# Performance work log

Measured on AMD Instinct MI355X. Metric: run time of the kernel, lower is better.

The kernel has to match this reference:

```python
import jax, jax.numpy as jnp
import numpy as np

D_MODEL = 512
D_ATTN = 128


def setup_inputs() -> dict:
    key = jax.random.key(0)
    k1, k2, k3, k4, k5 = jax.random.split(key, 5)
    B, N = 4, 4096
    x = jax.random.normal(k1, (B, N, D_MODEL), dtype=jnp.float32)
    key_mask = jnp.ones((B, N, 1), dtype=jnp.float32)
    # nn.Linear params (stored as [in, out] for x @ W)
    W_qkv = jax.random.normal(k2, (D_MODEL, 3 * D_ATTN), dtype=jnp.float32) / np.sqrt(D_MODEL)
    b_qkv = jax.random.normal(k3, (3 * D_ATTN,), dtype=jnp.float32) * 0.01
    W_out = jax.random.normal(k4, (D_ATTN, D_MODEL), dtype=jnp.float32) / np.sqrt(D_ATTN)
    b_out = jax.random.normal(k5, (D_MODEL,), dtype=jnp.float32) * 0.01
    return {"x": x, "key_mask": key_mask, "W_qkv": W_qkv, "b_qkv": b_qkv,
            "W_out": W_out, "b_out": b_out}


def reference(x, key_mask, W_qkv, b_qkv, W_out, b_out):
    # Fused QKV projection: [B, N, 3*d_attn]
    qkv = jnp.einsum('bnd,de->bne', x, W_qkv) + b_qkv
    q, k, v = jnp.split(qkv, 3, axis=-1)  # each [B, N, d_attn]
    d_attn = q.shape[-1]
    scale = 1.0 / np.sqrt(d_attn)
    # Full [B, N, N] score matrix (faithful to original einsum)
    scores = jnp.einsum('bnd,bmd->bnm', q, k)
    # Causal mask applied BEFORE scaling (as in original: mask, then *scale)
    N = x.shape[1]
    causal = jnp.tril(jnp.ones((N, N), dtype=bool))  # True = keep
    scores = jnp.where(causal[None, :, :], scores, -jnp.inf)
    scores = scores * scale
    attn = jax.nn.softmax(scores, axis=-1)  # dropout is identity in eval
    out = jnp.einsum('bnm,bmd->bnd', attn, v)
    out = out * key_mask  # broadcast [B, N, 1]
    out = jnp.einsum('bnd,de->bne', out, W_out) + b_out
    return out
```

## Files before the change

### kernel.cpp

```cpp
#include <hip/hip_runtime.h>
#include <hip/hip_bf16.h>
#include <math.h>

typedef __attribute__((ext_vector_type(4))) float f32x4;
typedef __attribute__((ext_vector_type(4))) float fvec4;
typedef __attribute__((ext_vector_type(8))) short bf16x8_t;
typedef __attribute__((ext_vector_type(4))) short bf16x4_t;

static constexpr int BATCH = 4;
static constexpr int SEQ = 4096;
static constexpr int DM = 512;
static constexpr int DA = 128;
static constexpr int BN = BATCH * SEQ;
static constexpr int IPB = 442;
static constexpr int N_ITEMS = BATCH * IPB;

static __device__ __forceinline__ unsigned short f2bf(float f) {
  unsigned u = __builtin_bit_cast(unsigned, f);
  u += 0x7fffu + ((u >> 16) & 1u);
  return (unsigned short)(u >> 16);
}
static __device__ __forceinline__ float bf2f(unsigned short u) {
  return __builtin_bit_cast(float, ((unsigned)u) << 16);
}
static __device__ __forceinline__ float fexp2(float x) {
#if __has_builtin(__builtin_amdgcn_exp2f)
  return __builtin_amdgcn_exp2f(x);
#else
  return exp2f(x);
#endif
}
static __device__ __forceinline__ unsigned pkbf(float lo, float hi) {
  unsigned r;
  asm("v_cvt_pk_bf16_f32 %0, %1, %2" : "=v"(r) : "v"(lo), "v"(hi));
  return r;
}

#define GLDS16(gsrc, ldst)                                                        \
  __builtin_amdgcn_global_load_lds(                                               \
      (const __attribute__((address_space(1))) void*)(gsrc),                      \
      (__attribute__((address_space(3))) void*)(ldst), 16, 0, 0)

static constexpr float QSC = 0.08838834764831845f * 1.4426950408889634f;

__global__ __launch_bounds__(256) void prep_kernel(
    const float* __restrict__ x, const float* __restrict__ Wqkv,
    const float* __restrict__ Wout, unsigned short* __restrict__ xbf,
    unsigned short* __restrict__ WqT, unsigned short* __restrict__ WoT) {
  long long i = ((long long)blockIdx.x * 256 + threadIdx.x) * 8;
  if (i < (long long)BN * DM) {
    fvec4 a = *(const fvec4*)&x[i];
    fvec4 b = *(const fvec4*)&x[i + 4];
    union { bf16x8_t v; unsigned short u[8]; } pk;
    pk.u[0] = f2bf(a[0]); pk.u[1] = f2bf(a[1]); pk.u[2] = f2bf(a[2]); pk.u[3] = f2bf(a[3]);
    pk.u[4] = f2bf(b[0]); pk.u[5] = f2bf(b[1]); pk.u[6] = f2bf(b[2]); pk.u[7] = f2bf(b[3]);
    *(bf16x8_t*)&xbf[i] = pk.v;
  }
  int t = blockIdx.x * 256 + threadIdx.x;
  if (t < 512 * 384) {
    int k = t / 384, n = t - k * 384;
    WqT[n * 512 + k] = f2bf(Wqkv[t]);
  }
  if (t < 128 * 512) {
    int k = t >> 9, n = t & 511;
    WoT[n * 128 + k] = f2bf(Wout[t]);
  }
}

__global__ __launch_bounds__(512, 4) void qkv_kernel(
    const unsigned short* __restrict__ xbf, const unsigned short* __restrict__ WqT,
    const float* __restrict__ bias, unsigned short* __restrict__ qbf,
    unsigned short* __restrict__ kpk, unsigned short* __restrict__ vpk) {
  __shared__ unsigned short Alds[128 * 64];
  __shared__ unsigned short Blds[128 * 64];

  const int m0 = blockIdx.x * 128;
  const int n0 = blockIdx.y * 128;
  const int tid = threadIdx.x;
  const int wave = tid >> 6, lane = tid & 63;
  const int g = lane >> 4, lr = lane & 15;
  const int wm = wave >> 2, wn = wave & 3;

  const int srow = lane >> 3;
  const int sslot = lane & 7;
  const int sksw = ((sslot ^ srow) * 8);

  f32x4 acc[4][2] = {};

  for (int kb = 0; kb < DM; kb += 64) {
    __syncthreads();
#pragma unroll
    for (int i = 0; i < 2; ++i) {
      int ch = wave * 2 + i;
      GLDS16(&xbf[(size_t)(m0 + ch * 8 + srow) * DM + kb + sksw],
             (char*)Alds + ch * 1024);
      GLDS16(&WqT[(size_t)(n0 + ch * 8 + srow) * DM + kb + sksw],
             (char*)Blds + ch * 1024);
    }
    asm volatile("s_waitcnt vmcnt(0)" ::: "memory");
    __syncthreads();

#pragma unroll
    for (int c2 = 0; c2 < 2; ++c2) {
      bf16x8_t ar[4], br[2];
#pragma unroll
      for (int mi = 0; mi < 4; ++mi) {
        int row = wm * 64 + mi * 16 + lr;
        ar[mi] = *(const bf16x8_t*)&Alds[row * 64 + (((c2 * 4 + g) ^ (row & 7)) * 8)];
      }
#pragma unroll
      for (int ni = 0; ni < 2; ++ni) {
        int row = wn * 32 + ni * 16 + lr;
        br[ni] = *(const bf16x8_t*)&Blds[row * 64 + (((c2 * 4 + g) ^ (row & 7)) * 8)];
      }
#pragma unroll
      for (int mi = 0; mi < 4; ++mi)
#pragma unroll
        for (int ni = 0; ni < 2; ++ni)
          acc[mi][ni] = __builtin_amdgcn_mfma_f32_16x16x32_bf16(ar[mi], br[ni],
                                                                acc[mi][ni], 0, 0, 0);
    }
  }

  if (n0 == 0) {
#pragma unroll
    for (int ni = 0; ni < 2; ++ni) {
      int col = wn * 32 + ni * 16 + lr;
      float bv = bias[col];
#pragma unroll
      for (int mi = 0; mi < 4; ++mi) {
        int tokb = m0 + wm * 64 + mi * 16 + 4 * g;
#pragma unroll
        for (int r = 0; r < 4; ++r)
          qbf[(size_t)(tokb + r) * DA + col] = f2bf((acc[mi][ni][r] + bv) * QSC);
      }
    }
  } else if (n0 == 128) {
#pragma unroll
    for (int ni = 0; ni < 2; ++ni) {
      int kd = wn * 32 + ni * 16 + lr;
      float bv = bias[128 + kd];
      int unit = (kd >> 5) * 4 + ((kd >> 3) & 3);
      int elem = kd & 7;
#pragma unroll
      for (int mi = 0; mi < 4; ++mi) {
        int tokb = m0 + wm * 64 + mi * 16 + 4 * g;
#pragma unroll
        for (int r = 0; r < 4; ++r) {
          int token = tokb + r;
          int tile32 = token >> 5;
          int u = (((token >> 4) & 1) * 16) + unit;
          kpk[(size_t)tile32 * 4096 + u * 128 + (token & 15) * 8 + elem] =
              f2bf(acc[mi][ni][r] + bv);
        }
      }
    }
  } else {
#pragma unroll
    for (int mi = 0; mi < 4; ++mi) {
      int keyb = m0 + wm * 64 + mi * 16 + 4 * g;
      int tile32 = keyb >> 5;
      int kl0 = keyb & 31;
      int gp = (kl0 >> 2) & 3;
      int jhi = kl0 >> 4;
#pragma unroll
      for (int ni = 0; ni < 2; ++ni) {
        int d = wn * 32 + ni * 16 + lr;
        float bv = bias[256 + d];
        union { bf16x4_t v; unsigned short u[4]; } pk;
#pragma unroll
        for (int r = 0; r < 4; ++r) pk.u[r] = f2bf(acc[mi][ni][r] + bv);
        int unit = (d >> 4) * 4 + gp;
        *(bf16x4_t*)&vpk[(size_t)tile32 * 4096 + unit * 128 + (d & 15) * 8 + jhi * 4] =
            pk.v;
      }
    }
  }
}

__global__ __launch_bounds__(256, 5) void attn_kernel(
    const unsigned short* __restrict__ qbf, const unsigned short* __restrict__ kpk,
    const unsigned short* __restrict__ vpk, const float* __restrict__ key_mask,
    unsigned short* __restrict__ part_o, float* __restrict__ part_ml,
    unsigned short* __restrict__ ctx) {
  __shared__ unsigned short KV[2][8192];

  const int flat = blockIdx.x;
  const int b = flat & 3;
  const int idxr = flat >> 2;
  int rem = idxr;
  int qt = 63;
  for (;;) {
    int nc = (qt + 5) / 5;
    if (rem < nc) break;
    rem -= nc;
    --qt;
  }
  const int ci = rem;
  const bool direct = (qt < 5);
  const int key0 = ci * 320;
  const int nkeys = min(320, (qt + 1) * 64 - key0);
  const int nt = nkeys >> 5;

  const int tid = threadIdx.x;
  const int wave = tid >> 6, lane = tid & 63;
  const int g = lane >> 4, lr = lane & 15;
  const int qloc = wave * 16 + lr;

  bf16x8_t qf[4];
  {
    const unsigned short* qb =
        qbf + ((size_t)(b * SEQ + qt * 64 + qloc)) * DA + g * 8;
#pragma unroll
    for (int c = 0; c < 4; ++c) qf[c] = *(const bf16x8_t*)(qb + c * 32);
  }

  f32x4 oacc[8] = {};
  float m_r = -INFINITY, l_r = 0.f;

  const int t32b = b * 128 + ci * 10;
  const unsigned short* ksrc = kpk + (size_t)t32b * 4096 + wave * 1024 + lane * 8;
  const unsigned short* vsrc = vpk + (size_t)t32b * 4096 + wave * 1024 + lane * 8;

#define STAGE(buf, tt)                                                       \
  do {                                                                       \
    char* kd_ = (char*)&KV[buf][0] + wave * 2048;                            \
    char* vd_ = (char*)&KV[buf][4096] + wave * 2048;                         \
    _Pragma("unroll")                                                        \
    for (int i_ = 0; i_ < 2; ++i_) {                                         \
      GLDS16(ksrc + (size_t)(tt) * 4096 + i_ * 512, kd_ + i_ * 1024);        \
      GLDS16(vsrc + (size_t)(tt) * 4096 + i_ * 512, vd_ + i_ * 1024);        \
    }                                                                        \
  } while (0)

  STAGE(0, 0);

  for (int tt = 0; tt < nt; ++tt) {
    const int cur = tt & 1;
    if (tt + 1 < nt) {
      STAGE(cur ^ 1, tt + 1);
      asm volatile("s_waitcnt vmcnt(4)" ::: "memory");
    } else {
      asm volatile("s_waitcnt vmcnt(0)" ::: "memory");
    }
    __builtin_amdgcn_s_barrier();
    __builtin_amdgcn_sched_barrier(0);

    f32x4 sacc[2] = {};
    __builtin_amdgcn_s_setprio(1);
#pragma unroll
    for (int ct = 0; ct < 2; ++ct)
#pragma unroll
      for (int c = 0; c < 4; ++c) {
        bf16x8_t kf = *(const bf16x8_t*)&KV[cur][((ct * 16 + c * 4 + g) * 16 + lr) * 8];
        sacc[ct] = __builtin_amdgcn_mfma_f32_16x16x32_bf16(kf, qf[c], sacc[ct], 0, 0, 0);
      }
    __builtin_amdgcn_s_setprio(0);

    const int koff = key0 + tt * 32 - qt * 64;
    if (koff + 31 > wave * 16) {
      int thr = qloc - koff;
#pragma unroll
      for (int ct = 0; ct < 2; ++ct)
#pragma unroll
        for (int r = 0; r < 4; ++r)
          if (16 * ct + 4 * g + r > thr) sacc[ct][r] = -INFINITY;
    }

    float tmax = fmaxf(fmaxf(fmaxf(sacc[0][0], sacc[0][1]), fmaxf(sacc[0][2], sacc[0][3])),
                       fmaxf(fmaxf(sacc[1][0], sacc[1][1]), fmaxf(sacc[1][2], sacc[1][3])));
    tmax = fmaxf(tmax, __shfl_xor(tmax, 16, 64));
    tmax = fmaxf(tmax, __shfl_xor(tmax, 32, 64));

    if (!__all(tmax <= m_r + 10.0f)) {
      float mn = fmaxf(m_r, tmax);
      float al = fexp2(m_r - mn);
      m_r = mn;
      l_r *= al;
#pragma unroll
      for (int t = 0; t < 8; ++t)
#pragma unroll
        for (int r = 0; r < 4; ++r) oacc[t][r] *= al;
    }

    float rs = 0.f;
#pragma unroll
    for (int ct = 0; ct < 2; ++ct)
#pragma unroll
      for (int r = 0; r < 4; ++r) {
        float p = fexp2(sacc[ct][r] - m_r);
        sacc[ct][r] = p;
        rs += p;
      }
    rs += __shfl_xor(rs, 16, 64);
    rs += __shfl_xor(rs, 32, 64);
    l_r += rs;

    bf16x8_t pb;
    {
      union { unsigned u[4]; bf16x8_t v; } pk;
      pk.u[0] = pkbf(sacc[0][0], sacc[0][1]);
      pk.u[1] = pkbf(sacc[0][2], sacc[0][3]);
      pk.u[2] = pkbf(sacc[1][0], sacc[1][1]);
      pk.u[3] = pkbf(sacc[1][2], sacc[1][3]);
      pb = pk.v;
    }

    __builtin_amdgcn_s_setprio(1);
#pragma unroll
    for (int t = 0; t < 8; ++t) {
      bf16x8_t vf = *(const bf16x8_t*)&KV[cur][4096 + ((t * 4 + g) * 16 + lr) * 8];
      oacc[t] = __builtin_amdgcn_mfma_f32_16x16x32_bf16(vf, pb, oacc[t], 0, 0, 0);
    }
    __builtin_amdgcn_s_setprio(0);

    __builtin_amdgcn_s_barrier();
  }
#undef STAGE

  const int row = qloc;
  if (direct) {
    float km = key_mask[b * SEQ + qt * 64 + row];
    float inv = km / l_r;
    unsigned short* co = ctx + ((size_t)(b * SEQ + qt * 64 + row)) * DA;
#pragma unroll
    for (int t = 0; t < 8; ++t) {
      union { bf16x4_t v; unsigned short u[4]; } pk;
#pragma unroll
      for (int r = 0; r < 4; ++r) pk.u[r] = f2bf(oacc[t][r] * inv);
      *(bf16x4_t*)&co[t * 16 + 4 * g] = pk.v;
    }
  } else {
    const int slot = b * IPB + idxr;
    unsigned short* po = part_o + (size_t)slot * 8192 + row * 128;
#pragma unroll
    for (int t = 0; t < 8; ++t) {
      union { bf16x4_t v; unsigned short u[4]; } pk;
#pragma unroll
      for (int r = 0; r < 4; ++r) pk.u[r] = f2bf(oacc[t][r]);
      *(bf16x4_t*)&po[t * 16 + 4 * g] = pk.v;
    }
    if (g == 0) {
      float2 ml = make_float2(m_r, l_r);
      *(float2*)&part_ml[((size_t)slot * 64 + row) * 2] = ml;
    }
  }
}

__global__ __launch_bounds__(256) void combine_kernel(
    const unsigned short* __restrict__ part_o, const float* __restrict__ part_ml,
    const float* __restrict__ key_mask, unsigned short* __restrict__ ctx) {
  const int qt = 5 + blockIdx.x;
  const int b = blockIdx.y;
  const int nc = (qt + 5) / 5;
  int idx0 = 0;
  for (int q = 63; q > qt; --q) idx0 += (q + 5) / 5;
  const int row = threadIdx.x >> 2, cg = threadIdx.x & 3;

  float m = -INFINITY;
  for (int ci = 0; ci < nc; ++ci) {
    int slot = b * IPB + idx0 + ci;
    m = fmaxf(m, part_ml[((size_t)slot * 64 + row) * 2 + 0]);
  }
  float l = 0.f;
  float acc[32];
#pragma unroll
  for (int k = 0; k < 32; ++k) acc[k] = 0.f;
  for (int ci = 0; ci < nc; ++ci) {
    int slot = b * IPB + idx0 + ci;
    float mi = part_ml[((size_t)slot * 64 + row) * 2 + 0];
    float li = part_ml[((size_t)slot * 64 + row) * 2 + 1];
    float w = fexp2(mi - m);
    l += w * li;
    const unsigned short* po = part_o + (size_t)slot * 8192 + row * 128 + cg * 32;
#pragma unroll
    for (int k8 = 0; k8 < 4; ++k8) {
      bf16x8_t v = *(const bf16x8_t*)(po + k8 * 8);
#pragma unroll
      for (int jj = 0; jj < 8; ++jj)
        acc[k8 * 8 + jj] += w * bf2f((unsigned short)v[jj]);
    }
  }
  int rowg = (b * 64 + qt) * 64 + row;
  float sc = key_mask[rowg] / l;
  unsigned short* co = ctx + (size_t)rowg * 128 + cg * 32;
#pragma unroll
  for (int k8 = 0; k8 < 4; ++k8) {
    union { bf16x8_t v; unsigned short u[8]; } pk;
#pragma unroll
    for (int jj = 0; jj < 8; ++jj) pk.u[jj] = f2bf(acc[k8 * 8 + jj] * sc);
    *(bf16x8_t*)(co + k8 * 8) = pk.v;
  }
}

__global__ __launch_bounds__(256) void outproj_kernel(
    const unsigned short* __restrict__ ctx, const unsigned short* __restrict__ WoT,
    const float* __restrict__ bias, float* __restrict__ out) {
  __shared__ unsigned short Alds[64 * 32];
  __shared__ unsigned short Blds[64 * 32];

  const int m0 = blockIdx.x * 64;
  const int n0 = blockIdx.y * 64;
  const int tid = threadIdx.x;
  const int wave = tid >> 6, lane = tid & 63;
  const int g = lane >> 4, lr = lane & 15;
  const int sar = tid >> 2, sak = tid & 3;
  const int sbc = tid & 63, sbk = tid >> 6;

  f32x4 acc[4] = {};

  for (int kb = 0; kb < DA; kb += 32) {
    __syncthreads();
    {
      bf16x8_t v = *(const bf16x8_t*)&ctx[(size_t)(m0 + sar) * DA + kb + sak * 8];
      *(bf16x8_t*)&Alds[(((sar >> 4) * 4 + sak) * 16 + (sar & 15)) * 8] = v;
    }
    {
      bf16x8_t v = *(const bf16x8_t*)&WoT[(size_t)(n0 + sbc) * DA + kb + sbk * 8];
      *(bf16x8_t*)&Blds[(((sbc >> 4) * 4 + sbk) * 16 + (sbc & 15)) * 8] = v;
    }
    __syncthreads();
    bf16x8_t af = *(const bf16x8_t*)&Alds[((wave * 4 + g) * 16 + lr) * 8];
#pragma unroll
    for (int c = 0; c < 4; ++c) {
      bf16x8_t bfr = *(const bf16x8_t*)&Blds[((c * 4 + g) * 16 + lr) * 8];
      acc[c] = __builtin_amdgcn_mfma_f32_16x16x32_bf16(af, bfr, acc[c], 0, 0, 0);
    }
  }

  const int rowb = m0 + wave * 16 + g * 4;
#pragma unroll
  for (int c = 0; c < 4; ++c) {
    int col = n0 + c * 16 + lr;
    float bv = bias[col];
#pragma unroll
    for (int r = 0; r < 4; ++r)
      out[(size_t)(rowb + r) * DM + col] = acc[c][r] + bv;
  }
}

extern "C" void kernel_launch(void* const* d_in, const int* in_sizes, int n_in,
                              void* d_out, int out_size, void* d_ws, size_t ws_size,
                              hipStream_t stream) {
  const float* x = (const float*)d_in[0];
  const float* key_mask = (const float*)d_in[1];
  const float* W_qkv = (const float*)d_in[2];
  const float* b_qkv = (const float*)d_in[3];
  const float* W_out = (const float*)d_in[4];
  const float* b_out = (const float*)d_in[5];
  float* out = (float*)d_out;

  unsigned short* ws = (unsigned short*)d_ws;
  unsigned short* qbf = ws;
  unsigned short* kpk = qbf + (size_t)BN * DA;
  unsigned short* vpk = kpk + (size_t)BN * DA;
  unsigned short* ctx = vpk + (size_t)BN * DA;
  unsigned short* xbf = ctx + (size_t)BN * DA;
  unsigned short* WqT = xbf + (size_t)BN * DM;
  unsigned short* WoT = WqT + (size_t)384 * 512;
  unsigned short* part_o = WoT + (size_t)512 * 128;
  float* part_ml = (float*)(part_o + (size_t)N_ITEMS * 8192);

  prep_kernel<<<dim3((BN * DM / 8 + 255) / 256), 256, 0, stream>>>(
      x, W_qkv, W_out, xbf, WqT, WoT);
  qkv_kernel<<<dim3(BN / 128, 3), 512, 0, stream>>>(xbf, WqT, b_qkv, qbf, kpk, vpk);
  attn_kernel<<<dim3(N_ITEMS), 256, 0, stream>>>(qbf, kpk, vpk, key_mask,
                                                 part_o, part_ml, ctx);
  combine_kernel<<<dim3(59, 4), 256, 0, stream>>>(part_o, part_ml, key_mask, ctx);
  outproj_kernel<<<dim3(BN / 64, 8), 256, 0, stream>>>(ctx, WoT, b_out, out);
}
```

Before: 89.79 us.

## Process 128 queries per attention block to reuse each staged K/V tile

Each attention workgroup now handles two 64-row query groups (128 queries), so every K/V tile staged into LDS feeds twice as many MFMAs. The split-K work items, partial buffers and combine kernel are resized to match. Mask values switch from -inf to large finite constants so fully masked rows stay finite. The aim is to halve K/V global and LDS traffic per unit of work. In exchange, register pressure doubles, occupancy drops (launch bounds 5 to 2), and there are fewer, larger work items, which may balance poorly across CUs.

```diff
diff --git a/kernel.cpp b/kernel.cpp
--- a/kernel.cpp
+++ b/kernel.cpp
@@ -12,8 +12,11 @@
 static constexpr int DM = 512;
 static constexpr int DA = 128;
 static constexpr int BN = BATCH * SEQ;
-static constexpr int IPB = 442;
+static constexpr int IPB = 224;
 static constexpr int N_ITEMS = BATCH * IPB;
+
+static constexpr float MASKV = -3.0e38f;
+static constexpr float MINIT = -1.0e30f;
 
 static __device__ __forceinline__ unsigned short f2bf(float f) {
   unsigned u = __builtin_bit_cast(unsigned, f);
@@ -178,7 +181,43 @@
   }
 }
 
-__global__ __launch_bounds__(256, 5) void attn_kernel(
+static __device__ __forceinline__ bf16x8_t softmax_grp(
+    f32x4 s[2], float& m_r, float& l_r, f32x4* oacc) {
+  float tmax = fmaxf(fmaxf(fmaxf(s[0][0], s[0][1]), fmaxf(s[0][2], s[0][3])),
+                     fmaxf(fmaxf(s[1][0], s[1][1]), fmaxf(s[1][2], s[1][3])));
+  tmax = fmaxf(tmax, __shfl_xor(tmax, 16, 64));
+  tmax = fmaxf(tmax, __shfl_xor(tmax, 32, 64));
+  if (!__all(tmax <= m_r + 10.0f)) {
+    float mn = fmaxf(m_r, tmax);
+    float al = fexp2(m_r - mn);
+    m_r = mn;
+    l_r *= al;
+#pragma unroll
+    for (int t = 0; t < 8; ++t)
+#pragma unroll
+      for (int r = 0; r < 4; ++r) oacc[t][r] *= al;
+  }
+  float rs = 0.f;
+#pragma unroll
+  for (int ct = 0; ct < 2; ++ct)
+#pragma unroll
+    for (int r = 0; r < 4; ++r) {
+      float p = fexp2(s[ct][r] - m_r);
+      s[ct][r] = p;
+      rs += p;
+    }
+  rs += __shfl_xor(rs, 16, 64);
+  rs += __shfl_xor(rs, 32, 64);
+  l_r += rs;
+  union { unsigned u[4]; bf16x8_t v; } pk;
+  pk.u[0] = pkbf(s[0][0], s[0][1]);
+  pk.u[1] = pkbf(s[0][2], s[0][3]);
+  pk.u[2] = pkbf(s[1][0], s[1][1]);
+  pk.u[3] = pkbf(s[1][2], s[1][3]);
+  return pk.v;
+}
+
+__global__ __launch_bounds__(256, 2) void attn_kernel(
     const unsigned short* __restrict__ qbf, const unsigned short* __restrict__ kpk,
     const unsigned short* __restrict__ vpk, const float* __restrict__ key_mask,
     unsigned short* __restrict__ part_o, float* __restrict__ part_ml,
@@ -189,34 +228,37 @@
   const int b = flat & 3;
   const int idxr = flat >> 2;
   int rem = idxr;
-  int qt = 63;
+  int qb = 31;
   for (;;) {
-    int nc = (qt + 5) / 5;
+    int nc = (2 * (qb + 1) + 4) / 5;
     if (rem < nc) break;
     rem -= nc;
-    --qt;
+    --qb;
   }
   const int ci = rem;
-  const bool direct = (qt < 5);
+  const bool direct = (qb < 2);
   const int key0 = ci * 320;
-  const int nkeys = min(320, (qt + 1) * 64 - key0);
+  const int nkeys = min(320, (qb + 1) * 128 - key0);
   const int nt = nkeys >> 5;
 
   const int tid = threadIdx.x;
   const int wave = tid >> 6, lane = tid & 63;
   const int g = lane >> 4, lr = lane & 15;
-  const int qloc = wave * 16 + lr;
-
-  bf16x8_t qf[4];
+  const int q0 = wave * 16 + lr;
+  const int q1 = q0 + 64;
+
+  bf16x8_t qf0[4], qf1[4];
   {
-    const unsigned short* qb =
-        qbf + ((size_t)(b * SEQ + qt * 64 + qloc)) * DA + g * 8;
-#pragma unroll
-    for (int c = 0; c < 4; ++c) qf[c] = *(const bf16x8_t*)(qb + c * 32);
-  }
-
-  f32x4 oacc[8] = {};
-  float m_r = -INFINITY, l_r = 0.f;
+    const unsigned short* qbase = qbf + ((size_t)(b * SEQ + qb * 128)) * DA + g * 8;
+#pragma unroll
+    for (int c = 0; c < 4; ++c) {
+      qf0[c] = *(const bf16x8_t*)(qbase + (size_t)q0 * DA + c * 32);
+      qf1[c] = *(const bf16x8_t*)(qbase + (size_t)q1 * DA + c * 32);
+    }
+  }
+
+  f32x4 oacc0[8] = {}, oacc1[8] = {};
+  float m0r = MINIT, l0 = 0.f, m1r = MINIT, l1 = 0.f;
 
   const int t32b = b * 128 + ci * 10;
   const unsigned short* ksrc = kpk + (size_t)t32b * 4096 + wave * 1024 + lane * 8;
@@ -246,71 +288,45 @@
     __builtin_amdgcn_s_barrier();
     __builtin_amdgcn_sched_barrier(0);
 
-    f32x4 sacc[2] = {};
+    f32x4 s0[2] = {}, s1[2] = {};
     __builtin_amdgcn_s_setprio(1);
 #pragma unroll
     for (int ct = 0; ct < 2; ++ct)
 #pragma unroll
       for (int c = 0; c < 4; ++c) {
         bf16x8_t kf = *(const bf16x8_t*)&KV[cur][((ct * 16 + c * 4 + g) * 16 + lr) * 8];
-        sacc[ct] = __builtin_amdgcn_mfma_f32_16x16x32_bf16(kf, qf[c], sacc[ct], 0, 0, 0);
+        s0[ct] = __builtin_amdgcn_mfma_f32_16x16x32_bf16(kf, qf0[c], s0[ct], 0, 0, 0);
+        s1[ct] = __builtin_amdgcn_mfma_f32_16x16x32_bf16(kf, qf1[c], s1[ct], 0, 0, 0);
       }
     __builtin_amdgcn_s_setprio(0);
 
-    const int koff = key0 + tt * 32 - qt * 64;
+    const int koff = key0 + tt * 32 - qb * 128;
     if (koff + 31 > wave * 16) {
-      int thr = qloc - koff;
+      int thr = q0 - koff;
 #pragma unroll
       for (int ct = 0; ct < 2; ++ct)
 #pragma unroll
         for (int r = 0; r < 4; ++r)
-          if (16 * ct + 4 * g + r > thr) sacc[ct][r] = -INFINITY;
-    }
-
-    float tmax = fmaxf(fmaxf(fmaxf(sacc[0][0], sacc[0][1]), fmaxf(sacc[0][2], sacc[0][3])),
-                       fmaxf(fmaxf(sacc[1][0], sacc[1][1]), fmaxf(sacc[1][2], sacc[1][3])));
-    tmax = fmaxf(tmax, __shfl_xor(tmax, 16, 64));
-    tmax = fmaxf(tmax, __shfl_xor(tmax, 32, 64));
-
-    if (!__all(tmax <= m_r + 10.0f)) {
-      float mn = fmaxf(m_r, tmax);
-      float al = fexp2(m_r - mn);
-      m_r = mn;
-      l_r *= al;
-#pragma unroll
-      for (int t = 0; t < 8; ++t)
-#pragma unroll
-        for (int r = 0; r < 4; ++r) oacc[t][r] *= al;
-    }
-
-    float rs = 0.f;
-#pragma unroll
-    for (int ct = 0; ct < 2; ++ct)
-#pragma unroll
-      for (int r = 0; r < 4; ++r) {
-        float p = fexp2(sacc[ct][r] - m_r);
-        sacc[ct][r] = p;
-        rs += p;
-      }
-    rs += __shfl_xor(rs, 16, 64);
-    rs += __shfl_xor(rs, 32, 64);
-    l_r += rs;
-
-    bf16x8_t pb;
-    {
-      union { unsigned u[4]; bf16x8_t v; } pk;
-      pk.u[0] = pkbf(sacc[0][0], sacc[0][1]);
-      pk.u[1] = pkbf(sacc[0][2], sacc[0][3]);
-      pk.u[2] = pkbf(sacc[1][0], sacc[1][1]);
-      pk.u[3] = pkbf(sacc[1][2], sacc[1][3]);
-      pb = pk.v;
-    }
+          if (16 * ct + 4 * g + r > thr) s0[ct][r] = MASKV;
+    }
+    if (koff + 31 > 64 + wave * 16) {
+      int thr = q1 - koff;
+#pragma unroll
+      for (int ct = 0; ct < 2; ++ct)
+#pragma unroll
+        for (int r = 0; r < 4; ++r)
+          if (16 * ct + 4 * g + r > thr) s1[ct][r] = MASKV;
+    }
+
+    bf16x8_t pb0 = softmax_grp(s0, m0r, l0, oacc0);
+    bf16x8_t pb1 = softmax_grp(s1, m1r, l1, oacc1);
 
     __builtin_amdgcn_s_setprio(1);
 #pragma unroll
     for (int t = 0; t < 8; ++t) {
       bf16x8_t vf = *(const bf16x8_t*)&KV[cur][4096 + ((t * 4 + g) * 16 + lr) * 8];
-      oacc[t] = __builtin_amdgcn_mfma_f32_16x16x32_bf16(vf, pb, oacc[t], 0, 0, 0);
+      oacc0[t] = __builtin_amdgcn_mfma_f32_16x16x32_bf16(vf, pb0, oacc0[t], 0, 0, 0);
+      oacc1[t] = __builtin_amdgcn_mfma_f32_16x16x32_bf16(vf, pb1, oacc1[t], 0, 0, 0);
     }
     __builtin_amdgcn_s_setprio(0);
 
@@ -318,49 +334,55 @@
   }
 #undef STAGE
 
-  const int row = qloc;
-  if (direct) {
-    float km = key_mask[b * SEQ + qt * 64 + row];
-    float inv = km / l_r;
-    unsigned short* co = ctx + ((size_t)(b * SEQ + qt * 64 + row)) * DA;
-#pragma unroll
-    for (int t = 0; t < 8; ++t) {
-      union { bf16x4_t v; unsigned short u[4]; } pk;
-#pragma unroll
-      for (int r = 0; r < 4; ++r) pk.u[r] = f2bf(oacc[t][r] * inv);
-      *(bf16x4_t*)&co[t * 16 + 4 * g] = pk.v;
-    }
-  } else {
-    const int slot = b * IPB + idxr;
-    unsigned short* po = part_o + (size_t)slot * 8192 + row * 128;
-#pragma unroll
-    for (int t = 0; t < 8; ++t) {
-      union { bf16x4_t v; unsigned short u[4]; } pk;
-#pragma unroll
-      for (int r = 0; r < 4; ++r) pk.u[r] = f2bf(oacc[t][r]);
-      *(bf16x4_t*)&po[t * 16 + 4 * g] = pk.v;
-    }
-    if (g == 0) {
-      float2 ml = make_float2(m_r, l_r);
-      *(float2*)&part_ml[((size_t)slot * 64 + row) * 2] = ml;
-    }
-  }
-}
-
-__global__ __launch_bounds__(256) void combine_kernel(
+  const int slot = b * IPB + idxr;
+#pragma unroll
+  for (int grp = 0; grp < 2; ++grp) {
+    const int row = grp ? q1 : q0;
+    const f32x4* oa = grp ? oacc1 : oacc0;
+    const float mr = grp ? m1r : m0r;
+    const float lr_ = grp ? l1 : l0;
+    if (direct) {
+      float km = key_mask[b * SEQ + qb * 128 + row];
+      float inv = km / lr_;
+      unsigned short* co = ctx + ((size_t)(b * SEQ + qb * 128 + row)) * DA;
+#pragma unroll
+      for (int t = 0; t < 8; ++t) {
+        union { bf16x4_t v; unsigned short u[4]; } pk;
+#pragma unroll
+        for (int r = 0; r < 4; ++r) pk.u[r] = f2bf(oa[t][r] * inv);
+        *(bf16x4_t*)&co[t * 16 + 4 * g] = pk.v;
+      }
+    } else {
+      unsigned short* po = part_o + (size_t)slot * 16384 + (size_t)row * 128;
+#pragma unroll
+      for (int t = 0; t < 8; ++t) {
+        union { bf16x4_t v; unsigned short u[4]; } pk;
+#pragma unroll
+        for (int r = 0; r < 4; ++r) pk.u[r] = f2bf(oa[t][r]);
+        *(bf16x4_t*)&po[t * 16 + 4 * g] = pk.v;
+      }
+      if (g == 0) {
+        float2 ml = make_float2(mr, lr_);
+        *(float2*)&part_ml[((size_t)slot * 128 + row) * 2] = ml;
+      }
+    }
+  }
+}
+
+__global__ __launch_bounds__(512) void combine_kernel(
     const unsigned short* __restrict__ part_o, const float* __restrict__ part_ml,
     const float* __restrict__ key_mask, unsigned short* __restrict__ ctx) {
-  const int qt = 5 + blockIdx.x;
+  const int qb = 2 + blockIdx.x;
   const int b = blockIdx.y;
-  const int nc = (qt + 5) / 5;
+  const int nc = (2 * (qb + 1) + 4) / 5;
   int idx0 = 0;
-  for (int q = 63; q > qt; --q) idx0 += (q + 5) / 5;
+  for (int q = 31; q > qb; --q) idx0 += (2 * (q + 1) + 4) / 5;
   const int row = threadIdx.x >> 2, cg = threadIdx.x & 3;
 
-  float m = -INFINITY;
+  float m = MINIT;
   for (int ci = 0; ci < nc; ++ci) {
     int slot = b * IPB + idx0 + ci;
-    m = fmaxf(m, part_ml[((size_t)slot * 64 + row) * 2 + 0]);
+    m = fmaxf(m, part_ml[((size_t)slot * 128 + row) * 2 + 0]);
   }
   float l = 0.f;
   float acc[32];
@@ -368,11 +390,11 @@
   for (int k = 0; k < 32; ++k) acc[k] = 0.f;
   for (int ci = 0; ci < nc; ++ci) {
     int slot = b * IPB + idx0 + ci;
-    float mi = part_ml[((size_t)slot * 64 + row) * 2 + 0];
-    float li = part_ml[((size_t)slot * 64 + row) * 2 + 1];
+    float mi = part_ml[((size_t)slot * 128 + row) * 2 + 0];
+    float li = part_ml[((size_t)slot * 128 + row) * 2 + 1];
     float w = fexp2(mi - m);
     l += w * li;
-    const unsigned short* po = part_o + (size_t)slot * 8192 + row * 128 + cg * 32;
+    const unsigned short* po = part_o + (size_t)slot * 16384 + (size_t)row * 128 + cg * 32;
 #pragma unroll
     for (int k8 = 0; k8 < 4; ++k8) {
       bf16x8_t v = *(const bf16x8_t*)(po + k8 * 8);
@@ -381,7 +403,7 @@
         acc[k8 * 8 + jj] += w * bf2f((unsigned short)v[jj]);
     }
   }
-  int rowg = (b * 64 + qt) * 64 + row;
+  int rowg = b * SEQ + qb * 128 + row;
   float sc = key_mask[rowg] / l;
   unsigned short* co = ctx + (size_t)rowg * 128 + cg * 32;
 #pragma unroll
@@ -459,13 +481,13 @@
   unsigned short* WqT = xbf + (size_t)BN * DM;
   unsigned short* WoT = WqT + (size_t)384 * 512;
   unsigned short* part_o = WoT + (size_t)512 * 128;
-  float* part_ml = (float*)(part_o + (size_t)N_ITEMS * 8192);
+  float* part_ml = (float*)(part_o + (size_t)N_ITEMS * 16384);
 
   prep_kernel<<<dim3((BN * DM / 8 + 255) / 256), 256, 0, stream>>>(
       x, W_qkv, W_out, xbf, WqT, WoT);
   qkv_kernel<<<dim3(BN / 128, 3), 512, 0, stream>>>(xbf, WqT, b_qkv, qbf, kpk, vpk);
   attn_kernel<<<dim3(N_ITEMS), 256, 0, stream>>>(qbf, kpk, vpk, key_mask,
                                                  part_o, part_ml, ctx);
-  combine_kernel<<<dim3(59, 4), 256, 0, stream>>>(part_o, part_ml, key_mask, ctx);
+  combine_kernel<<<dim3(30, 4), 512, 0, stream>>>(part_o, part_ml, key_mask, ctx);
   outproj_kernel<<<dim3(BN / 64, 8), 256, 0, stream>>>(ctx, WoT, b_out, out);
 }
```

Measured after the change: 95.85 us. 6.7% more time.
